# Performance work log

Hardware: AMD Instinct MI355X
Metric: run time of the kernel (lower is better)

Reference implementation:

```python
import jax, jax.numpy as jnp
import numpy as np

B, L = 8, 512
D_MODEL, N_HEADS, N_LAYERS = 768, 12, 12
D_HEAD = D_MODEL // N_HEADS
D_FF = 4 * D_MODEL
NUM_LABELS = 1000
PATCH_DIM = 16 * 16 * 3
EPS = 1e-6


def setup_inputs() -> dict:
    key = jax.random.key(0)
    ks = jax.random.split(key, 24)
    d = D_MODEL

    def w(k, shape, fan_in):
        return (jax.random.normal(k, shape, jnp.float32) / np.sqrt(fan_in)).astype(jnp.float32)

    return {
        'patch': jax.random.normal(ks[0], (B, L, PATCH_DIM), jnp.float32),
        'box': jax.random.uniform(ks[1], (B, L, 4), jnp.float32),
        'patch_W': w(ks[2], (PATCH_DIM, d), PATCH_DIM),
        'patch_b': jnp.zeros((d,), jnp.float32),
        'box_W': w(ks[3], (d, d), d),
        'box_b': jnp.zeros((d,), jnp.float32),
        'Wq': w(ks[4], (N_LAYERS, d, d), d),
        'Wk': w(ks[5], (N_LAYERS, d, d), d),
        'Wv': w(ks[6], (N_LAYERS, d, d), d),
        'Wo': w(ks[7], (N_LAYERS, d, d), d),
        'attn_norm_w': jnp.ones((N_LAYERS, d), jnp.float32),
        'gate_W': w(ks[8], (N_LAYERS, d, D_FF), d),
        'hidden_W': w(ks[9], (N_LAYERS, d, D_FF), d),
        'ffn_out_W': w(ks[10], (N_LAYERS, D_FF, d), D_FF),
        'ffn_norm_w': jnp.ones((N_LAYERS, d), jnp.float32),
        'reward_norm_w': jnp.ones((d,), jnp.float32),
        'reward_W': w(ks[11], (d, 2), d),
        'reward_b': jnp.zeros((2,), jnp.float32),
        'label_norm_w': jnp.ones((d,), jnp.float32),
        'label_W': w(ks[12], (d, NUM_LABELS), d),
        'label_b': jnp.zeros((NUM_LABELS,), jnp.float32),
        'box_norm_w': jnp.ones((d,), jnp.float32),
        'boxh_W': w(ks[13], (d, 4), d),
        'boxh_b': jnp.zeros((4,), jnp.float32),
    }


def _rmsnorm(x, wgt):
    return x * jax.lax.rsqrt(jnp.mean(x * x, axis=-1, keepdims=True) + EPS) * wgt


def _rope(x, cos, sin):
    # x: [b, n, l, dh]; consecutive pairs form complex numbers (view_as_complex)
    xr, xi = x[..., 0::2], x[..., 1::2]
    out_r = xr * cos - xi * sin
    out_i = xr * sin + xi * cos
    return jnp.stack((out_r, out_i), axis=-1).reshape(x.shape)


def _forward(patch, box, patch_W, patch_b, box_W, box_b, Wq, Wk, Wv, Wo,
             attn_norm_w, gate_W, hidden_W, ffn_out_W, ffn_norm_w,
             reward_norm_w, reward_W, reward_b, label_norm_w, label_W, label_b,
             box_norm_w, boxh_W, boxh_b):
    b, l, _ = patch.shape
    d = D_MODEL
    # StackedSinusoidalEmbedding(d_model, 4): d_stack = d/4, theta over d_stack/2 freqs
    d_stack = d // 4
    theta_box = 1.0 / (10000.0 ** (2.0 * jnp.arange(d_stack // 2, dtype=jnp.float32) / d_stack))
    ang = box[..., None] * theta_box  # [b, l, 4, d_stack/2]
    box_sin = jnp.stack((jnp.cos(ang), jnp.sin(ang)), axis=-1).reshape(b, l, d)

    x = (patch @ patch_W + patch_b) + (box_sin @ box_W + box_b)

    # RoPE tables and causal mask (constants)
    theta = 1.0 / (10000.0 ** (2.0 * jnp.arange(D_HEAD // 2, dtype=jnp.float32) / D_HEAD))
    pos_ang = jnp.arange(l, dtype=jnp.float32)[:, None] * theta  # [l, dh/2]
    cos, sin = jnp.cos(pos_ang), jnp.sin(pos_ang)
    mask = jnp.triu(jnp.full((l, l), -jnp.inf, dtype=jnp.float32), 1)
    scale = jnp.float32(np.sqrt(D_HEAD))

    def block(h, p):
        wq, wk, wv, wo, anw, gw, hw, ow, fnw = p
        hn = _rmsnorm(h, anw)
        q = (hn @ wq).reshape(b, l, N_HEADS, D_HEAD).transpose(0, 2, 1, 3)
        k = (hn @ wk).reshape(b, l, N_HEADS, D_HEAD).transpose(0, 2, 1, 3)
        v = (hn @ wv).reshape(b, l, N_HEADS, D_HEAD).transpose(0, 2, 1, 3)
        scores = jnp.einsum('bnld,bnmd->bnlm', _rope(q, cos, sin), _rope(k, cos, sin)) / scale
        attn = jax.nn.softmax(scores + mask, axis=-1)
        o = jnp.einsum('bnlm,bnmd->bnld', attn, v).transpose(0, 2, 1, 3).reshape(b, l, d)
        h = h + o @ wo
        hn = _rmsnorm(h, fnw)
        h = h + (jax.nn.silu(hn @ gw) * (hn @ hw)) @ ow
        return h, None

    x, _ = jax.lax.scan(block, x, (Wq, Wk, Wv, Wo, attn_norm_w, gate_W, hidden_W, ffn_out_W, ffn_norm_w))

    reward = _rmsnorm(x, reward_norm_w) @ reward_W + reward_b
    label = _rmsnorm(x, label_norm_w) @ label_W + label_b
    box_out = _rmsnorm(x, box_norm_w) @ boxh_W + boxh_b
    return reward, label, box_out


def reference(patch, box, patch_W, patch_b, box_W, box_b, Wq, Wk, Wv, Wo,
              attn_norm_w, gate_W, hidden_W, ffn_out_W, ffn_norm_w,
              reward_norm_w, reward_W, reward_b, label_norm_w, label_W, label_b,
              box_norm_w, boxh_W, boxh_b):
    return _forward(patch, box, patch_W, patch_b, box_W, box_b, Wq, Wk, Wv, Wo,
                    attn_norm_w, gate_W, hidden_W, ffn_out_W, ffn_norm_w,
                    reward_norm_w, reward_W, reward_b, label_norm_w, label_W, label_b,
                    box_norm_w, boxh_W, boxh_b)
```

## Files before the change

kernel.cpp:

```cpp
#include <hip/hip_runtime.h>
#include <math.h>
#include <type_traits>

#define B_   8
#define L_   512
#define MTOK 4096
#define D_   768
#define NH_  12
#define DH_  64
#define DFF_ 3072
#define NL_  12

typedef unsigned short u16;
typedef __attribute__((ext_vector_type(4))) float f32x4;
typedef __attribute__((ext_vector_type(8))) short i16x8;
typedef __attribute__((ext_vector_type(8))) __bf16 b16x8;

template <typename A, typename = void>
struct PickFrag { using type = i16x8; };
template <typename A>
struct PickFrag<A, std::void_t<decltype(__builtin_amdgcn_mfma_f32_16x16x32_bf16(
    std::declval<A>(), std::declval<A>(), std::declval<f32x4>(), 0, 0, 0))>> {
  using type = A;
};
using frag_t = typename PickFrag<b16x8>::type;

#if __has_builtin(__builtin_amdgcn_global_load_lds)
#define HAS_GLDS 1
#else
#define HAS_GLDS 0
#endif

__device__ inline u16 f2bf(float f) {
    unsigned u = __float_as_uint(f);
    unsigned r = u + 0x7fffu + ((u >> 16) & 1u);
    return (u16)(r >> 16);
}
__device__ inline float bf2f(u16 b) { return __uint_as_float(((unsigned)b) << 16); }

__global__ void k_box_sin(u16* __restrict__ emb, const float* __restrict__ box) {
    int idx = blockIdx.x * blockDim.x + threadIdx.x;
    if (idx >= MTOK * D_) return;
    int t = idx / D_, d = idx % D_;
    int c = d / 192, r = d % 192, j = r >> 1;
    float theta = __expf(-(float)j * (9.210340371976184f / 96.0f));
    float ang = box[t * 4 + c] * theta;
    emb[(size_t)t * 1536 + 768 + d] = f2bf((r & 1) ? sinf(ang) : cosf(ang));
}

__global__ void k_cast(u16* __restrict__ emb, const float* __restrict__ in, int n4) {
    int i = blockIdx.x * blockDim.x + threadIdx.x;
    if (i >= n4) return;
    int t = i / 192, c4 = (i % 192) * 4;
    float4 v = *reinterpret_cast<const float4*>(in + (size_t)t * 768 + c4);
    unsigned lo = (unsigned)f2bf(v.x) | ((unsigned)f2bf(v.y) << 16);
    unsigned hi = (unsigned)f2bf(v.z) | ((unsigned)f2bf(v.w) << 16);
    *reinterpret_cast<uint2*>(emb + (size_t)t * 1536 + c4) = make_uint2(lo, hi);
}

__global__ void k_addb(float* __restrict__ dst, const float* __restrict__ a,
                       const float* __restrict__ b) {
    int i = blockIdx.x * blockDim.x + threadIdx.x;
    if (i < D_) dst[i] = a[i] + b[i];
}

__global__ __launch_bounds__(256) void k_convT(u16* __restrict__ dst,
                                               const float* __restrict__ src,
                                               int K, int N, int ld, int rs,
                                               int ro, int co) {
    __shared__ float t[32][33];
    int bn = blockIdx.x * 32;
    int bk = blockIdx.y * 32;
    int tx = threadIdx.x % 32, ty = threadIdx.x / 32;
    #pragma unroll
    for (int i = 0; i < 4; ++i) {
        int k = bk + ty + i * 8;
        int n = bn + tx;
        t[ty + i * 8][tx] = (n < N) ? src[(size_t)k * N + n] : 0.0f;
    }
    __syncthreads();
    #pragma unroll
    for (int i = 0; i < 4; ++i) {
        int n = bn + ty + i * 8;
        int k = bk + tx;
        dst[(size_t)(n * rs + ro) * ld + co + k] = f2bf(t[tx][ty + i * 8]);
    }
}

__global__ __launch_bounds__(256) void k_convT_qkv(u16* __restrict__ dst,
                                                   const float* __restrict__ s0,
                                                   const float* __restrict__ s1,
                                                   const float* __restrict__ s2) {
    __shared__ float t[32][33];
    const float* src = blockIdx.z == 0 ? s0 : (blockIdx.z == 1 ? s1 : s2);
    u16* d = dst + (size_t)blockIdx.z * 768 * 768;
    int bn = blockIdx.x * 32, bk = blockIdx.y * 32;
    int tx = threadIdx.x % 32, ty = threadIdx.x / 32;
    #pragma unroll
    for (int i = 0; i < 4; ++i)
        t[ty + i * 8][tx] = src[(size_t)(bk + ty + i * 8) * 768 + bn + tx];
    __syncthreads();
    #pragma unroll
    for (int i = 0; i < 4; ++i) {
        int n = bn + ty + i * 8, k = bk + tx;
        d[(size_t)n * 768 + k] = f2bf(t[tx][ty + i * 8]);
    }
}

__global__ __launch_bounds__(256) void k_convT_gh(u16* __restrict__ dst,
                                                  const float* __restrict__ g,
                                                  const float* __restrict__ h) {
    __shared__ float t[32][33];
    const float* src = blockIdx.z ? h : g;
    int ro = blockIdx.z * 16;
    int bn = blockIdx.x * 32, bk = blockIdx.y * 32;
    int tx = threadIdx.x % 32, ty = threadIdx.x / 32;
    #pragma unroll
    for (int i = 0; i < 4; ++i)
        t[ty + i * 8][tx] = src[(size_t)(bk + ty + i * 8) * 3072 + bn + tx];
    __syncthreads();
    #pragma unroll
    for (int i = 0; i < 4; ++i) {
        int n = bn + ty + i * 8, k = bk + tx;
        int row = ((n >> 4) << 5) + (n & 15) + ro;
        dst[(size_t)row * 768 + k] = f2bf(t[tx][ty + i * 8]);
    }
}

__global__ __launch_bounds__(256) void k_rmsnorm(u16* __restrict__ out,
                                                 const float* __restrict__ in,
                                                 const float* __restrict__ w) {
    int t = blockIdx.x;
    const float* x = in + (size_t)t * D_;
    float ss = 0.f;
    for (int i = threadIdx.x; i < D_; i += 256) { float v = x[i]; ss += v * v; }
    for (int off = 32; off > 0; off >>= 1) ss += __shfl_down(ss, off);
    __shared__ float red[4];
    int wid = threadIdx.x >> 6, lane = threadIdx.x & 63;
    if (lane == 0) red[wid] = ss;
    __syncthreads();
    float tot = red[0] + red[1] + red[2] + red[3];
    float inv = rsqrtf(tot / (float)D_ + 1e-6f);
    for (int i = threadIdx.x; i < D_; i += 256)
        out[(size_t)t * D_ + i] = f2bf(x[i] * inv * w[i]);
}

template <int S>
__global__ __launch_bounds__(256) void k_fused_rr(float* __restrict__ h,
                                                  const float* __restrict__ part,
                                                  u16* __restrict__ hn,
                                                  const float* __restrict__ w) {
    int t = blockIdx.x;
    size_t base = (size_t)t * D_;
    float x[3];
    float ss = 0.f;
    #pragma unroll
    for (int c = 0; c < 3; ++c) {
        int i = threadIdx.x + c * 256;
        float v = h[base + i];
        #pragma unroll
        for (int s = 0; s < S; ++s)
            v += part[(size_t)s * MTOK * D_ + base + i];
        x[c] = v;
        h[base + i] = v;
        ss += v * v;
    }
    for (int off = 32; off > 0; off >>= 1) ss += __shfl_down(ss, off);
    __shared__ float red[4];
    int wid = threadIdx.x >> 6, lane = threadIdx.x & 63;
    if (lane == 0) red[wid] = ss;
    __syncthreads();
    float tot = red[0] + red[1] + red[2] + red[3];
    float inv = rsqrtf(tot / (float)D_ + 1e-6f);
    #pragma unroll
    for (int c = 0; c < 3; ++c) {
        int i = threadIdx.x + c * 256;
        hn[base + i] = f2bf(x[c] * inv * w[i]);
    }
}

__global__ void k_rope_tab(float* __restrict__ tab) {
    int idx = blockIdx.x * blockDim.x + threadIdx.x;
    if (idx >= L_ * 32) return;
    int l = idx >> 5, j = idx & 31;
    float theta = __expf(-(float)j * (9.210340371976184f / 32.0f));
    float s, c;
    sincosf((float)l * theta, &s, &c);
    tab[idx * 2] = c;
    tab[idx * 2 + 1] = s;
}

__global__ __launch_bounds__(256) void k_qkvprep(u16* __restrict__ qh,
                                                 u16* __restrict__ kh,
                                                 u16* __restrict__ vT,
                                                 const u16* __restrict__ qkv,
                                                 const float* __restrict__ tab) {
    int bh = blockIdx.x, lb = blockIdx.y;
    int b = bh / NH_, hh = bh % NH_;
    int tid = threadIdx.x;
    int r = tid >> 3, c8 = (tid & 7) * 8;
    int l = lb * 32 + r;
    size_t rowbase = ((size_t)(b * L_ + l)) * 2304 + hh * 64 + c8;

    float2 cs[4];
    #pragma unroll
    for (int p = 0; p < 4; ++p)
        cs[p] = *reinterpret_cast<const float2*>(tab + ((size_t)l * 32 + (c8 >> 1) + p) * 2);

    {
        uint4 v4 = *reinterpret_cast<const uint4*>(qkv + rowbase);
        const u16* pv = reinterpret_cast<const u16*>(&v4);
        u16 out[8];
        #pragma unroll
        for (int p = 0; p < 4; ++p) {
            float xr = bf2f(pv[2 * p]), xi = bf2f(pv[2 * p + 1]);
            out[2 * p]     = f2bf((xr * cs[p].x - xi * cs[p].y) * 0.125f);
            out[2 * p + 1] = f2bf((xr * cs[p].y + xi * cs[p].x) * 0.125f);
        }
        *reinterpret_cast<uint4*>(qh + ((size_t)bh * L_ + l) * 64 + c8) =
            *reinterpret_cast<uint4*>(out);
    }
    {
        uint4 v4 = *reinterpret_cast<const uint4*>(qkv + rowbase + 768);
        const u16* pv = reinterpret_cast<const u16*>(&v4);
        u16 out[8];
        #pragma unroll
        for (int p = 0; p < 4; ++p) {
            float xr = bf2f(pv[2 * p]), xi = bf2f(pv[2 * p + 1]);
            out[2 * p]     = f2bf(xr * cs[p].x - xi * cs[p].y);
            out[2 * p + 1] = f2bf(xr * cs[p].y + xi * cs[p].x);
        }
        *reinterpret_cast<uint4*>(kh + ((size_t)bh * L_ + l) * 64 + c8) =
            *reinterpret_cast<uint4*>(out);
    }
    __shared__ u16 ts[64][40];
    {
        uint4 v4 = *reinterpret_cast<const uint4*>(qkv + rowbase + 1536);
        const u16* pv = reinterpret_cast<const u16*>(&v4);
        #pragma unroll
        for (int j = 0; j < 8; ++j) ts[c8 + j][r] = pv[j];
    }
    __syncthreads();
    {
        int d = tid >> 2, l0 = (tid & 3) * 8;
        uint4 o4 = *reinterpret_cast<const uint4*>(&ts[d][l0]);
        *reinterpret_cast<uint4*>(vT + ((size_t)bh * 64 + d) * L_ + lb * 32 + l0) = o4;
    }
}

template <int MODE>
__global__ __launch_bounds__(256) void k_gemm_bf16(void* __restrict__ Cp,
                                                   const u16* __restrict__ A,
                                                   const u16* __restrict__ BT,
                                                   const float* __restrict__ bias,
                                                   int K, int Nout, int ldC) {
    __shared__ u16 As[2][128 * 32];
    __shared__ u16 Bs[2][128 * 32];
    int tid = threadIdx.x;
    int wid = tid >> 6, lane = tid & 63;

    int nx = gridDim.x, ny = gridDim.y, nz = gridDim.z;
    int bid = ((blockIdx.z * ny) + blockIdx.y) * nx + blockIdx.x;
    int nwg = nx * ny * nz;
    int cpx = nwg >> 3;
    int swz = (bid & 7) * cpx + (bid >> 3);
    int sk  = swz / (nx * ny);
    int rem = swz % (nx * ny);
    int by = rem / nx, bx = rem % nx;
    int row0 = by * 128, col0 = bx * 128;
    int wr = wid >> 1, wc = wid & 1;

    int Klen = K / nz;
    int kbeg = sk * Klen;

    int c0 = wid * 128 + lane;
    int c1 = c0 + 64;
    int r0 = c0 >> 2, kc0 = (c0 & 3) * 8;
    int r1 = c1 >> 2, kc1 = (c1 & 3) * 8;
    const u16* gA0 = A  + (size_t)(row0 + r0) * K + kbeg + kc0;
    const u16* gA1 = A  + (size_t)(row0 + r1) * K + kbeg + kc1;
    const u16* gB0 = BT + (size_t)(col0 + r0) * K + kbeg + kc0;
    const u16* gB1 = BT + (size_t)(col0 + r1) * K + kbeg + kc1;

    auto stage = [&](int buf, int kt) {
#if HAS_GLDS
        __builtin_amdgcn_global_load_lds(
            (const __attribute__((address_space(1))) void*)(gA0 + kt),
            (__attribute__((address_space(3))) void*)&As[buf][c0 * 8], 16, 0, 0);
        __builtin_amdgcn_global_load_lds(
            (const __attribute__((address_space(1))) void*)(gA1 + kt),
            (__attribute__((address_space(3))) void*)&As[buf][c1 * 8], 16, 0, 0);
        __builtin_amdgcn_global_load_lds(
            (const __attribute__((address_space(1))) void*)(gB0 + kt),
            (__attribute__((address_space(3))) void*)&Bs[buf][c0 * 8], 16, 0, 0);
        __builtin_amdgcn_global_load_lds(
            (const __attribute__((address_space(1))) void*)(gB1 + kt),
            (__attribute__((address_space(3))) void*)&Bs[buf][c1 * 8], 16, 0, 0);
#else
        *reinterpret_cast<uint4*>(&As[buf][c0 * 8]) = *reinterpret_cast<const uint4*>(gA0 + kt);
        *reinterpret_cast<uint4*>(&As[buf][c1 * 8]) = *reinterpret_cast<const uint4*>(gA1 + kt);
        *reinterpret_cast<uint4*>(&Bs[buf][c0 * 8]) = *reinterpret_cast<const uint4*>(gB0 + kt);
        *reinterpret_cast<uint4*>(&Bs[buf][c1 * 8]) = *reinterpret_cast<const uint4*>(gB1 + kt);
#endif
    };

    f32x4 acc[4][4] = {};
    int lrow = lane & 15, lk = (lane >> 4) * 8;

    stage(0, 0);
    __syncthreads();
    int cur = 0;
    for (int kt = 0; kt < Klen; kt += 32) {
        if (kt + 32 < Klen) stage(cur ^ 1, kt + 32);
        frag_t af[4], bfr[4];
        #pragma unroll
        for (int m = 0; m < 4; ++m)
            af[m] = *reinterpret_cast<const frag_t*>(&As[cur][(wr * 64 + m * 16 + lrow) * 32 + lk]);
        #pragma unroll
        for (int n = 0; n < 4; ++n)
            bfr[n] = *reinterpret_cast<const frag_t*>(&Bs[cur][(wc * 64 + n * 16 + lrow) * 32 + lk]);
        #pragma unroll
        for (int m = 0; m < 4; ++m)
            #pragma unroll
            for (int n = 0; n < 4; ++n)
                acc[m][n] = __builtin_amdgcn_mfma_f32_16x16x32_bf16(af[m], bfr[n], acc[m][n], 0, 0, 0);
        __syncthreads();
        cur ^= 1;
    }

    int lcol = lane & 15, rb = (lane >> 4) * 4;
    if (MODE == 5) {
        #pragma unroll
        for (int m = 0; m < 4; ++m) {
            #pragma unroll
            for (int np = 0; np < 2; ++np) {
                int ocol = (col0 >> 1) + wc * 32 + np * 16 + lcol;
                #pragma unroll
                for (int e = 0; e < 4; ++e) {
                    int row = row0 + wr * 64 + m * 16 + rb + e;
                    float g = acc[m][2 * np][e], hv = acc[m][2 * np + 1][e];
                    float s = g / (1.0f + __expf(-g));
                    ((u16*)Cp)[(size_t)row * ldC + ocol] = f2bf(s * hv);
                }
            }
        }
        return;
    }

    float* Cpart = (MODE == 4)
        ? ((float*)Cp + (size_t)sk * (size_t)(ny * 128) * ldC) : (float*)Cp;
    #pragma unroll
    for (int m = 0; m < 4; ++m) {
        #pragma unroll
        for (int n = 0; n < 4; ++n) {
            int col = col0 + wc * 64 + n * 16 + lcol;
            if (col >= Nout) continue;
            #pragma unroll
            for (int e = 0; e < 4; ++e) {
                int row = row0 + wr * 64 + m * 16 + rb + e;
                float v = acc[m][n][e];
                size_t off = (size_t)row * ldC + col;
                if (MODE == 0) {
                    if (bias) v += bias[col];
                    ((float*)Cp)[off] = v;
                } else if (MODE == 3) {
                    ((u16*)Cp)[off] = f2bf(v);
                } else if (MODE == 4) {
                    Cpart[off] = v;
                }
            }
        }
    }
}

__global__ __launch_bounds__(256) void k_attn3(u16* __restrict__ o,
                                               const u16* __restrict__ qh,
                                               const u16* __restrict__ kh,
                                               const u16* __restrict__ vT) {
    int bh = blockIdx.x, qb = blockIdx.y;
    int b = bh / NH_, hh = bh % NH_;
    int tid = threadIdx.x, wid = tid >> 6, lane = tid & 63;
    __shared__ u16 Qs[64][72], Ks[64][72], Vs[64][72], Ps[64][72];

    #pragma unroll
    for (int i = 0; i < 2; ++i) {
        int idx = tid + i * 256;
        int r = idx >> 3, c8 = (idx & 7) * 8;
        uint4 v4 = *reinterpret_cast<const uint4*>(
            qh + ((size_t)bh * L_ + qb * 64 + r) * 64 + c8);
        *reinterpret_cast<uint4*>(&Qs[r][c8]) = v4;
    }
    __syncthreads();

    int lr = lane & 15, lg = lane >> 4;
    frag_t aq[2];
    #pragma unroll
    for (int kd = 0; kd < 2; ++kd)
        aq[kd] = *reinterpret_cast<const frag_t*>(&Qs[wid * 16 + lr][kd * 32 + lg * 8]);

    f32x4 accO[4] = {};
    float M[4], S[4];
    #pragma unroll
    for (int e = 0; e < 4; ++e) { M[e] = -INFINITY; S[e] = 0.f; }

    for (int kb = 0; kb <= qb; ++kb) {
        __syncthreads();
        #pragma unroll
        for (int i = 0; i < 2; ++i) {
            int idx = tid + i * 256;
            int r = idx >> 3, c8 = (idx & 7) * 8;
            *reinterpret_cast<uint4*>(&Ks[r][c8]) = *reinterpret_cast<const uint4*>(
                kh + ((size_t)bh * L_ + kb * 64 + r) * 64 + c8);
            *reinterpret_cast<uint4*>(&Vs[r][c8]) = *reinterpret_cast<const uint4*>(
                vT + ((size_t)bh * 64 + r) * L_ + kb * 64 + c8);
        }
        __syncthreads();

        f32x4 sv[4];
        #pragma unroll
        for (int ct = 0; ct < 4; ++ct) {
            frag_t bk0 = *reinterpret_cast<const frag_t*>(&Ks[ct * 16 + lr][lg * 8]);
            frag_t bk1 = *reinterpret_cast<const frag_t*>(&Ks[ct * 16 + lr][32 + lg * 8]);
            f32x4 z = {0.f, 0.f, 0.f, 0.f};
            z = __builtin_amdgcn_mfma_f32_16x16x32_bf16(aq[0], bk0, z, 0, 0, 0);
            sv[ct] = __builtin_amdgcn_mfma_f32_16x16x32_bf16(aq[1], bk1, z, 0, 0, 0);
        }

        bool diag = (kb == qb);
        float esc[4];
        #pragma unroll
        for (int e = 0; e < 4; ++e) {
            int qg = qb * 64 + wid * 16 + lg * 4 + e;
            float mx = -1e30f;
            #pragma unroll
            for (int ct = 0; ct < 4; ++ct) {
                float s = sv[ct][e];
                if (diag && (kb * 64 + ct * 16 + lr > qg)) s = -1e30f;
                sv[ct][e] = s;
                mx = fmaxf(mx, s);
            }
            #pragma unroll
            for (int msk = 8; msk; msk >>= 1) mx = fmaxf(mx, __shfl_xor(mx, msk));
            float newM = fmaxf(M[e], mx);
            float ps = 0.f;
            #pragma unroll
            for (int ct = 0; ct < 4; ++ct) {
                float p = __expf(sv[ct][e] - newM);
                sv[ct][e] = p;
                ps += p;
            }
            #pragma unroll
            for (int msk = 8; msk; msk >>= 1) ps += __shfl_xor(ps, msk);
            esc[e] = __expf(M[e] - newM);
            S[e] = S[e] * esc[e] + ps;
            M[e] = newM;
        }
        #pragma unroll
        for (int dt = 0; dt < 4; ++dt)
            #pragma unroll
            for (int e = 0; e < 4; ++e) accO[dt][e] *= esc[e];

        #pragma unroll
        for (int ct = 0; ct < 4; ++ct)
            #pragma unroll
            for (int e = 0; e < 4; ++e)
                Ps[wid * 16 + lg * 4 + e][ct * 16 + lr] = f2bf(sv[ct][e]);

        frag_t pa0 = *reinterpret_cast<const frag_t*>(&Ps[wid * 16 + lr][lg * 8]);
        frag_t pa1 = *reinterpret_cast<const frag_t*>(&Ps[wid * 16 + lr][32 + lg * 8]);
        #pragma unroll
        for (int dt = 0; dt < 4; ++dt) {
            frag_t bv0 = *reinterpret_cast<const frag_t*>(&Vs[dt * 16 + lr][lg * 8]);
            frag_t bv1 = *reinterpret_cast<const frag_t*>(&Vs[dt * 16 + lr][32 + lg * 8]);
            accO[dt] = __builtin_amdgcn_mfma_f32_16x16x32_bf16(pa0, bv0, accO[dt], 0, 0, 0);
            accO[dt] = __builtin_amdgcn_mfma_f32_16x16x32_bf16(pa1, bv1, accO[dt], 0, 0, 0);
        }
    }

    #pragma unroll
    for (int dt = 0; dt < 4; ++dt) {
        #pragma unroll
        for (int e = 0; e < 4; ++e) {
            int row = b * L_ + qb * 64 + wid * 16 + lg * 4 + e;
            o[(size_t)row * D_ + hh * 64 + dt * 16 + lr] = f2bf(accO[dt][e] / S[e]);
        }
    }
}

__global__ __launch_bounds__(256) void k_heads3(float* __restrict__ out_reward,
                                                float* __restrict__ out_box,
                                                const float* __restrict__ h,
                                                const float* __restrict__ rnw,
                                                const float* __restrict__ rW,
                                                const float* __restrict__ rb,
                                                const float* __restrict__ bnw,
                                                const float* __restrict__ bW,
                                                const float* __restrict__ bb) {
    int t = blockIdx.x;
    size_t base = (size_t)t * D_;
    float x[3];
    float ss = 0.f;
    #pragma unroll
    for (int c = 0; c < 3; ++c) {
        int i = threadIdx.x + c * 256;
        x[c] = h[base + i];
        ss += x[c] * x[c];
    }
    for (int off = 32; off > 0; off >>= 1) ss += __shfl_down(ss, off);
    __shared__ float red[4];
    int wid = threadIdx.x >> 6, lane = threadIdx.x & 63;
    if (lane == 0) red[wid] = ss;
    __syncthreads();
    float inv = rsqrtf((red[0] + red[1] + red[2] + red[3]) / (float)D_ + 1e-6f);

    float a[6] = {};
    #pragma unroll
    for (int c = 0; c < 3; ++c) {
        int i = threadIdx.x + c * 256;
        float xr = x[c] * inv;
        float xw = xr * rnw[i];
        a[0] += xw * rW[i * 2];
        a[1] += xw * rW[i * 2 + 1];
        float xb = xr * bnw[i];
        #pragma unroll
        for (int j = 0; j < 4; ++j) a[2 + j] += xb * bW[i * 4 + j];
    }
    #pragma unroll
    for (int j = 0; j < 6; ++j)
        for (int off = 32; off > 0; off >>= 1) a[j] += __shfl_down(a[j], off);
    __shared__ float red2[4][6];
    if (lane == 0)
        #pragma unroll
        for (int j = 0; j < 6; ++j) red2[wid][j] = a[j];
    __syncthreads();
    if (threadIdx.x < 6) {
        float s = red2[0][threadIdx.x] + red2[1][threadIdx.x] +
                  red2[2][threadIdx.x] + red2[3][threadIdx.x];
        if (threadIdx.x < 2) out_reward[(size_t)t * 2 + threadIdx.x] = s + rb[threadIdx.x];
        else                 out_box[(size_t)t * 4 + threadIdx.x - 2] = s + bb[threadIdx.x - 2];
    }
}

extern "C" void kernel_launch(void* const* d_in, const int* in_sizes, int n_in,
                              void* d_out, int out_size, void* d_ws, size_t ws_size,
                              hipStream_t stream) {
    const float* patch        = (const float*)d_in[0];
    const float* box          = (const float*)d_in[1];
    const float* patch_W      = (const float*)d_in[2];
    const float* patch_b      = (const float*)d_in[3];
    const float* box_W        = (const float*)d_in[4];
    const float* box_b        = (const float*)d_in[5];
    const float* Wq           = (const float*)d_in[6];
    const float* Wk           = (const float*)d_in[7];
    const float* Wv           = (const float*)d_in[8];
    const float* Wo           = (const float*)d_in[9];
    const float* attn_norm_w  = (const float*)d_in[10];
    const float* gate_W       = (const float*)d_in[11];
    const float* hidden_W     = (const float*)d_in[12];
    const float* ffn_out_W    = (const float*)d_in[13];
    const float* ffn_norm_w   = (const float*)d_in[14];
    const float* reward_norm_w= (const float*)d_in[15];
    const float* reward_W     = (const float*)d_in[16];
    const float* reward_b     = (const float*)d_in[17];
    const float* label_norm_w = (const float*)d_in[18];
    const float* label_W      = (const float*)d_in[19];
    const float* label_b      = (const float*)d_in[20];
    const float* box_norm_w   = (const float*)d_in[21];
    const float* boxh_W       = (const float*)d_in[22];
    const float* boxh_b       = (const float*)d_in[23];

    char* w = (char*)d_ws;
    auto alloc = [&](size_t bytes) { char* p = w; w += (bytes + 255) & ~(size_t)255; return p; };

    u16*  wqkv   = (u16*)alloc((size_t)2304 * 768 * 2);
    u16*  wo_l   = (u16*)alloc((size_t)768 * 768 * 2);
    u16*  wgh    = (u16*)alloc((size_t)6144 * 768 * 2);
    u16*  wfo    = (u16*)alloc((size_t)768 * 3072 * 2);
    u16*  wcat   = (u16*)alloc((size_t)768 * 1536 * 2);
    u16*  wlab   = (u16*)alloc((size_t)1024 * 768 * 2);
    float* bias_c= (float*)alloc((size_t)768 * 4);
    u16*  emb    = (u16*)alloc((size_t)MTOK * 1536 * 2);
    float* h     = (float*)alloc((size_t)MTOK * D_ * 4);
    u16*  hn_bf  = (u16*)alloc((size_t)MTOK * D_ * 2);
    u16*  qkv_bf = (u16*)alloc((size_t)MTOK * 2304 * 2);
    u16*  vT     = (u16*)alloc((size_t)MTOK * D_ * 2);
    float* tab   = (float*)alloc((size_t)L_ * 32 * 2 * 4);
    u16*  o_bf   = (u16*)alloc((size_t)MTOK * D_ * 2);
    u16*  ga_bf  = (u16*)alloc((size_t)MTOK * DFF_ * 2);
    float* part  = (float*)alloc((size_t)4 * MTOK * D_ * 4);

    u16* qh = emb;
    u16* kh = emb + (size_t)MTOK * 768;

    dim3 blk(256);

    k_convT<<<dim3(24, 24), blk, 0, stream>>>(wcat, patch_W, 768, 768, 1536, 1, 0, 0);
    k_convT<<<dim3(24, 24), blk, 0, stream>>>(wcat, box_W,   768, 768, 1536, 1, 0, 768);
    k_convT<<<dim3(32, 24), blk, 0, stream>>>(wlab, label_W, 768, 1000, 768, 1, 0, 0);
    k_addb<<<3, blk, 0, stream>>>(bias_c, patch_b, box_b);
    k_rope_tab<<<(L_ * 32 + 255) / 256, blk, 0, stream>>>(tab);
    k_cast<<<(MTOK * 768 / 4 + 255) / 256, blk, 0, stream>>>(emb, patch, MTOK * 768 / 4);
    k_box_sin<<<(MTOK * D_ + 255) / 256, blk, 0, stream>>>(emb, box);

    k_gemm_bf16<0><<<dim3(6, 32), blk, 0, stream>>>(h, emb, wcat, bias_c, 1536, 768, 768);
    k_rmsnorm<<<MTOK, blk, 0, stream>>>(hn_bf, h, attn_norm_w);

    for (int ly = 0; ly < NL_; ++ly) {
        const float* wq  = Wq + (size_t)ly * D_ * D_;
        const float* wk  = Wk + (size_t)ly * D_ * D_;
        const float* wv  = Wv + (size_t)ly * D_ * D_;
        const float* wo  = Wo + (size_t)ly * D_ * D_;
        const float* gw  = gate_W + (size_t)ly * D_ * DFF_;
        const float* hw  = hidden_W + (size_t)ly * D_ * DFF_;
        const float* ow  = ffn_out_W + (size_t)ly * DFF_ * D_;
        const float* fnw = ffn_norm_w + (size_t)ly * D_;
        const float* nxt = (ly + 1 < NL_) ? attn_norm_w + (size_t)(ly + 1) * D_
                                          : label_norm_w;

        k_convT_qkv<<<dim3(24, 24, 3), blk, 0, stream>>>(wqkv, wq, wk, wv);
        k_gemm_bf16<3><<<dim3(18, 32), blk, 0, stream>>>(qkv_bf, hn_bf, wqkv, nullptr, 768, 2304, 2304);
        k_qkvprep<<<dim3(96, 16), blk, 0, stream>>>(qh, kh, vT, qkv_bf, tab);
        k_attn3<<<dim3(96, 8), blk, 0, stream>>>(o_bf, qh, kh, vT);
        k_convT<<<dim3(24, 24), blk, 0, stream>>>(wo_l, wo, 768, 768, 768, 1, 0, 0);
        k_gemm_bf16<4><<<dim3(6, 32, 2), blk, 0, stream>>>(part, o_bf, wo_l, nullptr, 768, 768, 768);
        k_fused_rr<2><<<MTOK, blk, 0, stream>>>(h, part, hn_bf, fnw);

        k_convT_gh<<<dim3(96, 24, 2), blk, 0, stream>>>(wgh, gw, hw);
        k_gemm_bf16<5><<<dim3(48, 32), blk, 0, stream>>>(ga_bf, hn_bf, wgh, nullptr, 768, 6144, 3072);
        k_convT<<<dim3(24, 96), blk, 0, stream>>>(wfo, ow, 3072, 768, 3072, 1, 0, 0);
        k_gemm_bf16<4><<<dim3(6, 32, 4), blk, 0, stream>>>(part, ga_bf, wfo, nullptr, 3072, 768, 768);
        k_fused_rr<4><<<MTOK, blk, 0, stream>>>(h, part, hn_bf, nxt);
    }

    float* out_reward = (float*)d_out;
    float* out_label  = out_reward + (size_t)MTOK * 2;
    float* out_box    = out_label + (size_t)MTOK * 1000;

    k_gemm_bf16<0><<<dim3(8, 32), blk, 0, stream>>>(out_label, hn_bf, wlab, label_b, 768, 1000, 1000);
    k_heads3<<<MTOK, blk, 0, stream>>>(out_reward, out_box, h,
                                       reward_norm_w, reward_W, reward_b,
                                       box_norm_w, boxh_W, boxh_b);
}
```

Before: 2.528 ms.

## Hoist weight transposes out of layer loop and relax GEMM barrier waits

All per-layer weight transpose/bf16 conversions are moved out of the layer loop into four batched launches over all 12 layers, written into per-layer workspace buffers. This cuts 48 small kernel launches and lets the conversion run with more parallelism, at the cost of a larger workspace. Separately, the GEMM main loop replaces __syncthreads with explicit s_waitcnt vmcnt(4) plus raw barriers. The goal is to let the next tile's async global-to-LDS loads stay in flight while the current tile is consumed.

New measurement: 2.466 ms. 2.5% less time.

```diff
diff --git a/kernel.cpp b/kernel.cpp
--- a/kernel.cpp
+++ b/kernel.cpp
@@ -38,6 +38,12 @@
 }
 __device__ inline float bf2f(u16 b) { return __uint_as_float(((unsigned)b) << 16); }
 
+__device__ inline void bar_raw() {
+    asm volatile("" ::: "memory");
+    __builtin_amdgcn_s_barrier();
+    asm volatile("" ::: "memory");
+}
+
 __global__ void k_box_sin(u16* __restrict__ emb, const float* __restrict__ box) {
     int idx = blockIdx.x * blockDim.x + threadIdx.x;
     if (idx >= MTOK * D_) return;
@@ -87,13 +93,33 @@
     }
 }
 
+__global__ __launch_bounds__(256) void k_convT_b1(u16* __restrict__ dst,
+                                                  const float* __restrict__ src,
+                                                  int K, int N) {
+    __shared__ float t[32][33];
+    const float* s = src + (size_t)blockIdx.z * K * N;
+    u16* d = dst + (size_t)blockIdx.z * K * N;
+    int bn = blockIdx.x * 32, bk = blockIdx.y * 32;
+    int tx = threadIdx.x % 32, ty = threadIdx.x / 32;
+    #pragma unroll
+    for (int i = 0; i < 4; ++i)
+        t[ty + i * 8][tx] = s[(size_t)(bk + ty + i * 8) * N + bn + tx];
+    __syncthreads();
+    #pragma unroll
+    for (int i = 0; i < 4; ++i) {
+        int n = bn + ty + i * 8, k = bk + tx;
+        d[(size_t)n * K + k] = f2bf(t[tx][ty + i * 8]);
+    }
+}
+
 __global__ __launch_bounds__(256) void k_convT_qkv(u16* __restrict__ dst,
                                                    const float* __restrict__ s0,
                                                    const float* __restrict__ s1,
                                                    const float* __restrict__ s2) {
     __shared__ float t[32][33];
-    const float* src = blockIdx.z == 0 ? s0 : (blockIdx.z == 1 ? s1 : s2);
-    u16* d = dst + (size_t)blockIdx.z * 768 * 768;
+    int ly = blockIdx.z / 3, which = blockIdx.z % 3;
+    const float* src = (which == 0 ? s0 : (which == 1 ? s1 : s2)) + (size_t)ly * 768 * 768;
+    u16* d = dst + ((size_t)ly * 3 + which) * 768 * 768;
     int bn = blockIdx.x * 32, bk = blockIdx.y * 32;
     int tx = threadIdx.x % 32, ty = threadIdx.x / 32;
     #pragma unroll
@@ -111,8 +137,10 @@
                                                   const float* __restrict__ g,
                                                   const float* __restrict__ h) {
     __shared__ float t[32][33];
-    const float* src = blockIdx.z ? h : g;
-    int ro = blockIdx.z * 16;
+    int ly = blockIdx.z >> 1, which = blockIdx.z & 1;
+    const float* src = (which ? h : g) + (size_t)ly * 768 * 3072;
+    u16* d = dst + (size_t)ly * 6144 * 768;
+    int ro = which * 16;
     int bn = blockIdx.x * 32, bk = blockIdx.y * 32;
     int tx = threadIdx.x % 32, ty = threadIdx.x / 32;
     #pragma unroll
@@ -123,7 +151,7 @@
     for (int i = 0; i < 4; ++i) {
         int n = bn + ty + i * 8, k = bk + tx;
         int row = ((n >> 4) << 5) + (n & 15) + ro;
-        dst[(size_t)row * 768 + k] = f2bf(t[tx][ty + i * 8]);
+        d[(size_t)row * 768 + k] = f2bf(t[tx][ty + i * 8]);
     }
 }
 
@@ -308,10 +336,14 @@
     int lrow = lane & 15, lk = (lane >> 4) * 8;
 
     stage(0, 0);
-    __syncthreads();
     int cur = 0;
     for (int kt = 0; kt < Klen; kt += 32) {
-        if (kt + 32 < Klen) stage(cur ^ 1, kt + 32);
+        bool has_next = (kt + 32 < Klen);
+        if (has_next) stage(cur ^ 1, kt + 32);
+        if (has_next) asm volatile("s_waitcnt vmcnt(4) lgkmcnt(0)" ::: "memory");
+        else          asm volatile("s_waitcnt vmcnt(0) lgkmcnt(0)" ::: "memory");
+        __builtin_amdgcn_sched_barrier(0);
+        bar_raw();
         frag_t af[4], bfr[4];
         #pragma unroll
         for (int m = 0; m < 4; ++m)
@@ -324,7 +356,7 @@
             #pragma unroll
             for (int n = 0; n < 4; ++n)
                 acc[m][n] = __builtin_amdgcn_mfma_f32_16x16x32_bf16(af[m], bfr[n], acc[m][n], 0, 0, 0);
-        __syncthreads();
+        bar_raw();
         cur ^= 1;
     }
 
@@ -572,10 +604,10 @@
     char* w = (char*)d_ws;
     auto alloc = [&](size_t bytes) { char* p = w; w += (bytes + 255) & ~(size_t)255; return p; };
 
-    u16*  wqkv   = (u16*)alloc((size_t)2304 * 768 * 2);
-    u16*  wo_l   = (u16*)alloc((size_t)768 * 768 * 2);
-    u16*  wgh    = (u16*)alloc((size_t)6144 * 768 * 2);
-    u16*  wfo    = (u16*)alloc((size_t)768 * 3072 * 2);
+    u16*  wqkv_a = (u16*)alloc((size_t)NL_ * 2304 * 768 * 2);
+    u16*  wo_a   = (u16*)alloc((size_t)NL_ * 768 * 768 * 2);
+    u16*  wgh_a  = (u16*)alloc((size_t)NL_ * 6144 * 768 * 2);
+    u16*  wfo_a  = (u16*)alloc((size_t)NL_ * 768 * 3072 * 2);
     u16*  wcat   = (u16*)alloc((size_t)768 * 1536 * 2);
     u16*  wlab   = (u16*)alloc((size_t)1024 * 768 * 2);
     float* bias_c= (float*)alloc((size_t)768 * 4);
@@ -599,6 +631,10 @@
     k_convT<<<dim3(32, 24), blk, 0, stream>>>(wlab, label_W, 768, 1000, 768, 1, 0, 0);
     k_addb<<<3, blk, 0, stream>>>(bias_c, patch_b, box_b);
     k_rope_tab<<<(L_ * 32 + 255) / 256, blk, 0, stream>>>(tab);
+    k_convT_qkv<<<dim3(24, 24, 36), blk, 0, stream>>>(wqkv_a, Wq, Wk, Wv);
+    k_convT_b1<<<dim3(24, 24, 12), blk, 0, stream>>>(wo_a, Wo, 768, 768);
+    k_convT_gh<<<dim3(96, 24, 24), blk, 0, stream>>>(wgh_a, gate_W, hidden_W);
+    k_convT_b1<<<dim3(24, 96, 12), blk, 0, stream>>>(wfo_a, ffn_out_W, 3072, 768);
     k_cast<<<(MTOK * 768 / 4 + 255) / 256, blk, 0, stream>>>(emb, patch, MTOK * 768 / 4);
     k_box_sin<<<(MTOK * D_ + 255) / 256, blk, 0, stream>>>(emb, box);
 
@@ -606,28 +642,21 @@
     k_rmsnorm<<<MTOK, blk, 0, stream>>>(hn_bf, h, attn_norm_w);
 
     for (int ly = 0; ly < NL_; ++ly) {
-        const float* wq  = Wq + (size_t)ly * D_ * D_;
-        const float* wk  = Wk + (size_t)ly * D_ * D_;
-        const float* wv  = Wv + (size_t)ly * D_ * D_;
-        const float* wo  = Wo + (size_t)ly * D_ * D_;
-        const float* gw  = gate_W + (size_t)ly * D_ * DFF_;
-        const float* hw  = hidden_W + (size_t)ly * D_ * DFF_;
-        const float* ow  = ffn_out_W + (size_t)ly * DFF_ * D_;
+        const u16* wqkv = wqkv_a + (size_t)ly * 2304 * 768;
+        const u16* wo_l = wo_a   + (size_t)ly * 768 * 768;
+        const u16* wgh  = wgh_a  + (size_t)ly * 6144 * 768;
+        const u16* wfo  = wfo_a  + (size_t)ly * 768 * 3072;
         const float* fnw = ffn_norm_w + (size_t)ly * D_;
         const float* nxt = (ly + 1 < NL_) ? attn_norm_w + (size_t)(ly + 1) * D_
                                           : label_norm_w;
 
-        k_convT_qkv<<<dim3(24, 24, 3), blk, 0, stream>>>(wqkv, wq, wk, wv);
         k_gemm_bf16<3><<<dim3(18, 32), blk, 0, stream>>>(qkv_bf, hn_bf, wqkv, nullptr, 768, 2304, 2304);
         k_qkvprep<<<dim3(96, 16), blk, 0, stream>>>(qh, kh, vT, qkv_bf, tab);
         k_attn3<<<dim3(96, 8), blk, 0, stream>>>(o_bf, qh, kh, vT);
-        k_convT<<<dim3(24, 24), blk, 0, stream>>>(wo_l, wo, 768, 768, 768, 1, 0, 0);
         k_gemm_bf16<4><<<dim3(6, 32, 2), blk, 0, stream>>>(part, o_bf, wo_l, nullptr, 768, 768, 768);
         k_fused_rr<2><<<MTOK, blk, 0, stream>>>(h, part, hn_bf, fnw);
 
-        k_convT_gh<<<dim3(96, 24, 2), blk, 0, stream>>>(wgh, gw, hw);
         k_gemm_bf16<5><<<dim3(48, 32), blk, 0, stream>>>(ga_bf, hn_bf, wgh, nullptr, 768, 6144, 3072);
-        k_convT<<<dim3(24, 96), blk, 0, stream>>>(wfo, ow, 3072, 768, 3072, 1, 0, 0);
         k_gemm_bf16<4><<<dim3(6, 32, 4), blk, 0, stream>>>(part, ga_bf, wfo, nullptr, 3072, 768, 768);
         k_fused_rr<4><<<MTOK, blk, 0, stream>>>(h, part, hn_bf, nxt);
     }
```
